# Kernel tuning notes

Hardware: AMD Instinct MI355X
Metric: run time of the kernel (lower is better)

The kernel has to match this reference:

```python
import jax, jax.numpy as jnp
import numpy as np

N_NODES = 50000
N_EDGES = 300000
HEADS = 2
OUT_CH = 128
BN_EPS = 1e-5
NEG_SLOPE = 0.2


def _batchnorm(x, g, b):
    # training-mode BatchNorm1d: biased batch statistics
    mean = x.mean(axis=0)
    var = x.var(axis=0)
    return (x - mean) * jax.lax.rsqrt(var + BN_EPS) * g + b


def _gatv2(x, src, dst, edge_attr, Wl, bl, Wr, br, We, att, bias, concat):
    # PyG GATv2Conv, share_weights=False, aggr='add'
    n = x.shape[0]
    xl = (x @ Wl + bl).reshape(n, HEADS, OUT_CH)  # source messages
    xr = (x @ Wr + br).reshape(n, HEADS, OUT_CH)  # destination term
    ee = (edge_attr @ We).reshape(-1, HEADS, OUT_CH)
    s = jax.nn.leaky_relu(xl[src] + xr[dst] + ee, NEG_SLOPE)  # [E,H,C]
    alpha = jnp.einsum('ehc,hc->eh', s, att)  # [E,H]
    # segment softmax over edges grouped by destination node
    m = jax.ops.segment_max(alpha, dst, num_segments=n)
    a = jnp.exp(alpha - m[dst])
    den = jax.ops.segment_sum(a, dst, num_segments=n)
    a = a / (den[dst] + 1e-16)
    out = jax.ops.segment_sum(xl[src] * a[:, :, None], dst, num_segments=n)  # [N,H,C]
    out = out.reshape(n, HEADS * OUT_CH) if concat else out.mean(axis=1)
    return out + bias


def setup_inputs() -> dict:
    key = jax.random.key(0)
    ks = jax.random.split(key, 16)
    d = {}
    d['h'] = jax.random.normal(ks[0], (N_NODES, 5), jnp.float32)
    d['edge_index'] = jax.random.randint(ks[1], (2, N_EDGES), 0, N_NODES, jnp.int64)
    d['edge_weight'] = jax.random.uniform(ks[2], (N_EDGES, 1), jnp.float32)
    d['bn0_g'] = jnp.ones((5,), jnp.float32)
    d['bn0_b'] = jnp.zeros((5,), jnp.float32)
    d['bn1_g'] = jnp.ones((256,), jnp.float32)
    d['bn1_b'] = jnp.zeros((256,), jnp.float32)
    def lin(k, fan_in, fan_out):
        return jax.random.normal(k, (fan_in, fan_out), jnp.float32) * (1.0 / np.sqrt(fan_in))
    # conv1: in=5 -> heads*out=256, concat=True
    d['c1_Wl'] = lin(ks[3], 5, 256); d['c1_bl'] = jnp.zeros((256,), jnp.float32)
    d['c1_Wr'] = lin(ks[4], 5, 256); d['c1_br'] = jnp.zeros((256,), jnp.float32)
    d['c1_We'] = lin(ks[5], 1, 256)
    d['c1_att'] = jax.random.normal(ks[6], (HEADS, OUT_CH), jnp.float32) * 0.1
    d['c1_bias'] = jnp.zeros((256,), jnp.float32)
    # mu: in=256 -> 128, concat=False
    d['mu_Wl'] = lin(ks[7], 256, 256); d['mu_bl'] = jnp.zeros((256,), jnp.float32)
    d['mu_Wr'] = lin(ks[8], 256, 256); d['mu_br'] = jnp.zeros((256,), jnp.float32)
    d['mu_We'] = lin(ks[9], 1, 256)
    d['mu_att'] = jax.random.normal(ks[10], (HEADS, OUT_CH), jnp.float32) * 0.1
    d['mu_bias'] = jnp.zeros((128,), jnp.float32)
    # log_std: same shapes as mu
    d['ls_Wl'] = lin(ks[11], 256, 256); d['ls_bl'] = jnp.zeros((256,), jnp.float32)
    d['ls_Wr'] = lin(ks[12], 256, 256); d['ls_br'] = jnp.zeros((256,), jnp.float32)
    d['ls_We'] = lin(ks[13], 1, 256)
    d['ls_att'] = jax.random.normal(ks[14], (HEADS, OUT_CH), jnp.float32) * 0.1
    d['ls_bias'] = jnp.zeros((128,), jnp.float32)
    return d


def reference(h, edge_index, edge_weight, bn0_g, bn0_b, bn1_g, bn1_b,
              c1_Wl, c1_bl, c1_Wr, c1_br, c1_We, c1_att, c1_bias,
              mu_Wl, mu_bl, mu_Wr, mu_br, mu_We, mu_att, mu_bias,
              ls_Wl, ls_bl, ls_Wr, ls_br, ls_We, ls_att, ls_bias):
    src, dst = edge_index[0], edge_index[1]
    x = _batchnorm(h, bn0_g, bn0_b)
    x = _gatv2(x, src, dst, edge_weight, c1_Wl, c1_bl, c1_Wr, c1_br, c1_We, c1_att, c1_bias, concat=True)
    x = jax.nn.relu(_batchnorm(x, bn1_g, bn1_b))
    # dropout identity (eval / deterministic)
    mu = _gatv2(x, src, dst, edge_weight, mu_Wl, mu_bl, mu_Wr, mu_br, mu_We, mu_att, mu_bias, concat=False)
    log_std = _gatv2(x, src, dst, edge_weight, ls_Wl, ls_bl, ls_Wr, ls_br, ls_We, ls_att, ls_bias, concat=False)
    return (mu, log_std)
```

## Files before the change

kernel.cpp:

```cpp
#include <hip/hip_runtime.h>
#include <math.h>

#define N_NODES 50000
#define N_EDGES 300000
#define BN_EPS 1e-5f
#define NEG_SLOPE 0.2f

#define RB_COUNT 3128
#define SCAN_TILES 49

typedef short bf8v __attribute__((ext_vector_type(8)));
typedef float f4v __attribute__((ext_vector_type(4)));

__device__ inline unsigned short f2bf(float f) {
    union { float f; unsigned u; } c; c.f = f;
    unsigned r = c.u + 0x7fffu + ((c.u >> 16) & 1u);
    return (unsigned short)(r >> 16);
}
__device__ inline float bf2f(unsigned short u) {
    union { unsigned u; float f; } c; c.u = ((unsigned)u) << 16;
    return c.f;
}

__device__ inline void async_copy16(void* lds, const void* g) {
    __builtin_amdgcn_global_load_lds(
        (const __attribute__((address_space(1))) unsigned int*)g,
        (__attribute__((address_space(3))) unsigned int*)lds, 16, 0, 0);
}

__global__ void bn0_reduce(const float* __restrict__ h, float* __restrict__ acc ) {
    __shared__ float lds[4][10];
    int tid = threadIdx.x;
    int lane = tid & 63, wave = tid >> 6;
    float ls[5] = {0,0,0,0,0}, lq[5] = {0,0,0,0,0};
    for (int r = blockIdx.x * 256 + tid; r < N_NODES; r += 128 * 256) {
        #pragma unroll
        for (int k = 0; k < 5; k++) {
            float v = h[r*5 + k];
            ls[k] += v; lq[k] += v*v;
        }
    }
    #pragma unroll
    for (int k = 0; k < 5; k++) {
        #pragma unroll
        for (int m = 1; m <= 32; m <<= 1) {
            ls[k] += __shfl_xor(ls[k], m, 64);
            lq[k] += __shfl_xor(lq[k], m, 64);
        }
    }
    if (lane == 0) {
        #pragma unroll
        for (int k = 0; k < 5; k++) { lds[wave][k] = ls[k]; lds[wave][5+k] = lq[k]; }
    }
    __syncthreads();
    if (tid < 10) {
        float s = lds[0][tid] + lds[1][tid] + lds[2][tid] + lds[3][tid];
        atomicAdd(&acc[tid], s);
    }
}

__global__ void bn0_finalize(const float* __restrict__ acc, const float* __restrict__ g,
                             const float* __restrict__ b, float* __restrict__ ss) {
    int tid = threadIdx.x;
    if (tid < 5) {
        float mean = acc[tid] * (1.f / N_NODES);
        float var  = acc[5 + tid] * (1.f / N_NODES) - mean*mean;
        float sc = g[tid] * rsqrtf(var + BN_EPS);
        ss[tid]     = sc;
        ss[5 + tid] = b[tid] - mean * sc;
    }
}

__global__ void bn0_apply(const float* __restrict__ h, const float* __restrict__ ss,
                          float* __restrict__ x0) {
    int i = blockIdx.x * blockDim.x + threadIdx.x;
    if (i < N_NODES * 5) {
        int k = i % 5;
        x0[i] = h[i] * ss[k] + ss[5 + k];
    }
}

__global__ void edge_count(const int* __restrict__ dst, int* __restrict__ count) {
    int e = blockIdx.x * blockDim.x + threadIdx.x;
    if (e < N_EDGES) atomicAdd(&count[dst[e]], 1);
}

__global__ void local_scan(const int* __restrict__ count, int* __restrict__ offsets,
                           int* __restrict__ tileSum) {
    __shared__ int lds[1024];
    int tid = threadIdx.x;
    int i = blockIdx.x * 1024 + tid;
    int v = (i < N_NODES) ? count[i] : 0;
    lds[tid] = v;
    __syncthreads();
    #pragma unroll
    for (int off = 1; off < 1024; off <<= 1) {
        int t = (tid >= off) ? lds[tid - off] : 0;
        __syncthreads();
        lds[tid] += t;
        __syncthreads();
    }
    if (i < N_NODES) offsets[i] = lds[tid] - v;
    if (tid == 1023) tileSum[blockIdx.x] = lds[1023];
}

__global__ void tile_scan(const int* __restrict__ tileSum, int* __restrict__ tilePrefix,
                          int* __restrict__ offsets) {
    int lane = threadIdx.x;
    int v = (lane < SCAN_TILES) ? tileSum[lane] : 0;
    int inc = v;
    #pragma unroll
    for (int off = 1; off < 64; off <<= 1) {
        int t = __shfl_up(inc, off, 64);
        if (lane >= off) inc += t;
    }
    int excl = inc - v;
    if (lane < SCAN_TILES) tilePrefix[lane] = excl;
    if (lane == SCAN_TILES - 1) offsets[N_NODES] = inc;
}

__global__ void add_prefix(int* __restrict__ offsets, const int* __restrict__ tilePrefix,
                           int* __restrict__ cursor) {
    int i = blockIdx.x * 1024 + threadIdx.x;
    if (i < N_NODES) {
        int o = offsets[i] + tilePrefix[blockIdx.x];
        offsets[i] = o;
        cursor[i] = o;
    }
}

__global__ void edge_scatter(const int* __restrict__ dst, const int* __restrict__ src,
                             const float* __restrict__ ew, int* __restrict__ cursor,
                             int* __restrict__ srcp, float* __restrict__ ewp) {
    int e = blockIdx.x * blockDim.x + threadIdx.x;
    if (e < N_EDGES) {
        int pos = atomicAdd(&cursor[dst[e]], 1);
        srcp[pos] = src[e];
        ewp[pos] = ew[e];
    }
}

__global__ void gemm_k5(const float* __restrict__ x0,
                        const float* __restrict__ Wl, const float* __restrict__ bl,
                        const float* __restrict__ Wr, const float* __restrict__ br,
                        unsigned short* __restrict__ xl, unsigned short* __restrict__ xr) {
    int n = blockIdx.x;
    int c = threadIdx.x;
    float a0 = x0[n*5+0], a1 = x0[n*5+1], a2 = x0[n*5+2], a3 = x0[n*5+3], a4 = x0[n*5+4];
    float l = bl[c] + a0*Wl[c] + a1*Wl[256+c] + a2*Wl[512+c] + a3*Wl[768+c] + a4*Wl[1024+c];
    float r = br[c] + a0*Wr[c] + a1*Wr[256+c] + a2*Wr[512+c] + a3*Wr[768+c] + a4*Wr[1024+c];
    xl[n*256 + c] = f2bf(l);
    xr[n*256 + c] = f2bf(r);
}

__global__ void pack_x_bn(const float* __restrict__ x,
                          const float* __restrict__ sum, const float* __restrict__ sumsq,
                          const float* __restrict__ g, const float* __restrict__ b,
                          unsigned short* __restrict__ ap) {
    int t = blockIdx.x * 256 + threadIdx.x;
    int lane = t & 63;
    int kc = (t >> 6) & 7;
    int rb = t >> 9;
    int row = rb * 16 + (lane & 15);
    int k0 = kc * 32 + (lane >> 4) * 8;
    union { unsigned short h[8]; uint4 u; } tmp;
    if (row < N_NODES) {
        const float* s = x + (size_t)row * 256 + k0;
        #pragma unroll
        for (int j = 0; j < 8; j++) {
            int c = k0 + j;
            float mean = sum[c] * (1.f / N_NODES);
            float var  = sumsq[c] * (1.f / N_NODES) - mean*mean;
            float sc = g[c] * rsqrtf(var + BN_EPS);
            float v = (s[j] - mean) * sc + b[c];
            v = v > 0.f ? v : 0.f;
            tmp.h[j] = f2bf(v);
        }
    } else {
        #pragma unroll
        for (int j = 0; j < 8; j++) tmp.h[j] = 0;
    }
    *reinterpret_cast<uint4*>(ap + (size_t)t * 8) = tmp.u;
}

__global__ void pack_w(const float* __restrict__ Wl0, const float* __restrict__ Wr0,
                       const float* __restrict__ Wl1, const float* __restrict__ Wr1,
                       unsigned short* __restrict__ bp) {
    int t = blockIdx.x * 256 + threadIdx.x;
    int lane = t & 63;
    int nt = (t >> 6) & 31;
    int kc = (t >> 11) & 7;
    int conv = t >> 14;
    int col = nt * 16 + (lane & 15);
    int k0 = kc * 32 + (lane >> 4) * 8;
    const float* W = conv ? (col < 256 ? Wl1 : Wr1) : (col < 256 ? Wl0 : Wr0);
    int c = col & 255;
    union { unsigned short h[8]; uint4 u; } tmp;
    #pragma unroll
    for (int j = 0; j < 8; j++) tmp.h[j] = f2bf(W[(size_t)(k0 + j) * 256 + c]);
    *reinterpret_cast<uint4*>(bp + (size_t)t * 8) = tmp.u;
}

__global__ __launch_bounds__(512) void gemm_mfma(const unsigned short* __restrict__ ap,
        const unsigned short* __restrict__ bp,
        const float* __restrict__ bl, const float* __restrict__ br,
        unsigned short* __restrict__ xl, unsigned short* __restrict__ xr) {
    __shared__ unsigned short Bs[2][32][512];
    int lane = threadIdx.x & 63;
    int wave = threadIdx.x >> 6;
    int h = wave & 1;
    int rb = blockIdx.x * 4 + (wave >> 1);

    const unsigned short* aptr = ap + (size_t)rb * 4096 + lane * 8;
    const unsigned short* bsrc = bp + lane * 8;

    auto stage = [&](int buf, int kc) {
        #pragma unroll
        for (int j = 0; j < 4; j++) {
            int f = wave * 4 + j;
            async_copy16(&Bs[buf][f][lane * 8], bsrc + (size_t)kc * 16384 + f * 512);
        }
    };
    stage(0, 0);

    bf8v a[8];
    #pragma unroll
    for (int kc = 0; kc < 8; kc++) a[kc] = *reinterpret_cast<const bf8v*>(aptr + kc * 512);

    f4v acc[16];
    #pragma unroll
    for (int t = 0; t < 16; t++) acc[t] = (f4v){0.f, 0.f, 0.f, 0.f};

    for (int kc = 0; kc < 8; kc++) {
        __syncthreads();
        if (kc < 7) stage((kc + 1) & 1, kc + 1);
        const unsigned short* bb = &Bs[kc & 1][h * 16][lane * 8];
        #pragma unroll
        for (int t = 0; t < 16; t++) {
            bf8v b = *reinterpret_cast<const bf8v*>(bb + t * 512);
            acc[t] = __builtin_amdgcn_mfma_f32_16x16x32_bf16(a[kc], b, acc[t], 0, 0, 0);
        }
    }

    int c15 = lane & 15;
    int row0 = rb * 16 + (lane >> 4) * 4;
    unsigned short* outp = h ? xr : xl;
    const float* bias = h ? br : bl;
    #pragma unroll
    for (int t = 0; t < 16; t++) {
        int col = t * 16 + c15;
        float bv = bias[col];
        #pragma unroll
        for (int r = 0; r < 4; r++) {
            int row = row0 + r;
            if (row < N_NODES) outp[(size_t)row * 256 + col] = f2bf(acc[t][r] + bv);
        }
    }
}

template <int CONCAT>
__global__ void agg_fused(const unsigned short* __restrict__ xl,
                          const unsigned short* __restrict__ xr,
                          const float* __restrict__ We, const float* __restrict__ att,
                          const int* __restrict__ offsets, const int* __restrict__ srcp,
                          const float* __restrict__ ewp, const float* __restrict__ bias,
                          float* __restrict__ out) {
    int n = blockIdx.x * 4 + (threadIdx.x >> 6);
    int lane = threadIdx.x & 63;
    if (n >= N_NODES) return;
    int col = (lane >> 5) * 128 + (lane & 31) * 4;
    float4 w4 = *(const float4*)(We + col);
    float4 a4 = *(const float4*)(att + col);
    ushort4 r4 = *(const ushort4*)(xr + (size_t)n * 256 + col);
    float rx = bf2f(r4.x), ry = bf2f(r4.y), rz = bf2f(r4.z), rw = bf2f(r4.w);
    int beg = offsets[n], end = offsets[n + 1];
    float mrun = -INFINITY, den = 0.f;
    float ax = 0.f, ay = 0.f, az = 0.f, aw = 0.f;
    for (int i = beg; i < end; i++) {
        int s = srcp[i];
        float w = ewp[i];
        ushort4 l4 = *(const ushort4*)(xl + (size_t)s * 256 + col);
        float lx = bf2f(l4.x), ly = bf2f(l4.y), lz = bf2f(l4.z), lw = bf2f(l4.w);
        float v, a = 0.f;
        v = lx + rx + w*w4.x; v = v > 0.f ? v : NEG_SLOPE*v; a += v*a4.x;
        v = ly + ry + w*w4.y; v = v > 0.f ? v : NEG_SLOPE*v; a += v*a4.y;
        v = lz + rz + w*w4.z; v = v > 0.f ? v : NEG_SLOPE*v; a += v*a4.z;
        v = lw + rw + w*w4.w; v = v > 0.f ? v : NEG_SLOPE*v; a += v*a4.w;
        #pragma unroll
        for (int mm = 1; mm <= 16; mm <<= 1) a += __shfl_xor(a, mm, 64);
        float nm = fmaxf(mrun, a);
        float sc = __expf(mrun - nm);
        float p  = __expf(a - nm);
        den = den * sc + p;
        ax = ax * sc + p * lx;
        ay = ay * sc + p * ly;
        az = az * sc + p * lz;
        aw = aw * sc + p * lw;
        mrun = nm;
    }
    float inv = 1.f / (den + 1e-16f);
    if (CONCAT) {
        float4 b4 = *(const float4*)(bias + col);
        float4 o;
        o.x = ax*inv + b4.x; o.y = ay*inv + b4.y; o.z = az*inv + b4.z; o.w = aw*inv + b4.w;
        *(float4*)(out + (size_t)n * 256 + col) = o;
    } else {
        float ox = ax*inv, oy = ay*inv, oz = az*inv, ow = aw*inv;
        float px = __shfl_xor(ox, 32, 64);
        float py = __shfl_xor(oy, 32, 64);
        float pz = __shfl_xor(oz, 32, 64);
        float pw = __shfl_xor(ow, 32, 64);
        if (lane < 32) {
            float4 b4 = *(const float4*)(bias + lane * 4);
            float4 o;
            o.x = (ox + px)*0.5f + b4.x;
            o.y = (oy + py)*0.5f + b4.y;
            o.z = (oz + pz)*0.5f + b4.z;
            o.w = (ow + pw)*0.5f + b4.w;
            *(float4*)(out + (size_t)n * 128 + lane * 4) = o;
        }
    }
}

__global__ void bn1_reduce(const float* __restrict__ x, float* __restrict__ sum,
                           float* __restrict__ sumsq) {
    int c = threadIdx.x;
    int r0 = blockIdx.x * 196;
    int r1 = r0 + 196; if (r1 > N_NODES) r1 = N_NODES;
    float s = 0.f, q = 0.f;
    for (int r = r0; r < r1; r++) {
        float v = x[r*256 + c];
        s += v; q += v*v;
    }
    atomicAdd(&sum[c], s);
    atomicAdd(&sumsq[c], q);
}

extern "C" void kernel_launch(void* const* d_in, const int* in_sizes, int n_in,
                              void* d_out, int out_size, void* d_ws, size_t ws_size,
                              hipStream_t stream) {
    const float* h          = (const float*)d_in[0];
    const int*   edge_index = (const int*)d_in[1];
    const int*   src = edge_index;
    const int*   dst = edge_index + N_EDGES;
    const float* ew   = (const float*)d_in[2];
    const float* bn0g = (const float*)d_in[3];
    const float* bn0b = (const float*)d_in[4];
    const float* bn1g = (const float*)d_in[5];
    const float* bn1b = (const float*)d_in[6];
    const float* c1_Wl = (const float*)d_in[7];
    const float* c1_bl = (const float*)d_in[8];
    const float* c1_Wr = (const float*)d_in[9];
    const float* c1_br = (const float*)d_in[10];
    const float* c1_We = (const float*)d_in[11];
    const float* c1_att = (const float*)d_in[12];
    const float* c1_bias = (const float*)d_in[13];
    const float* mu_Wl = (const float*)d_in[14];
    const float* mu_bl = (const float*)d_in[15];
    const float* mu_Wr = (const float*)d_in[16];
    const float* mu_br = (const float*)d_in[17];
    const float* mu_We = (const float*)d_in[18];
    const float* mu_att = (const float*)d_in[19];
    const float* mu_bias = (const float*)d_in[20];
    const float* ls_Wl = (const float*)d_in[21];
    const float* ls_bl = (const float*)d_in[22];
    const float* ls_Wr = (const float*)d_in[23];
    const float* ls_br = (const float*)d_in[24];
    const float* ls_We = (const float*)d_in[25];
    const float* ls_att = (const float*)d_in[26];
    const float* ls_bias = (const float*)d_in[27];

    float* out_mu = (float*)d_out;
    float* out_ls = (float*)d_out + (size_t)N_NODES * 128;

    char* ws = (char*)d_ws;
    size_t off = 0;
    auto alloc = [&](size_t bytes) -> void* {
        void* p = ws + off;
        off += (bytes + 255) / 256 * 256;
        return p;
    };
    float* x0      = (float*)alloc((size_t)N_NODES * 5 * 4);
    unsigned short* xl = (unsigned short*)alloc((size_t)N_NODES * 256 * 2);
    unsigned short* xr = (unsigned short*)alloc((size_t)N_NODES * 256 * 2);
    float* xB      = (float*)alloc((size_t)N_NODES * 256 * 4);
    float* bn0acc  = (float*)alloc(10 * 4);
    float* bn0ss   = (float*)alloc(10 * 4);
    float* bn1sum  = (float*)alloc(256 * 4);
    float* bn1sq   = (float*)alloc(256 * 4);
    int*   count   = (int*)alloc((size_t)N_NODES * 4);
    int*   offsets = (int*)alloc((size_t)(N_NODES + 1) * 4);
    int*   cursor  = (int*)alloc((size_t)N_NODES * 4);
    int*   srcp    = (int*)alloc((size_t)N_EDGES * 4);
    float* ewp     = (float*)alloc((size_t)N_EDGES * 4);
    int*   tileSum = (int*)alloc((size_t)SCAN_TILES * 4);
    int*   tilePre = (int*)alloc((size_t)SCAN_TILES * 4);
    unsigned short* Apack = (unsigned short*)alloc((size_t)RB_COUNT * 4096 * 2);
    unsigned short* Bpack = (unsigned short*)alloc((size_t)2 * 131072 * 2);

    hipMemsetAsync(count, 0, (size_t)N_NODES * 4, stream);
    hipMemsetAsync(bn0acc, 0, 10 * 4, stream);
    hipMemsetAsync(bn1sum, 0, 256 * 4, stream);
    hipMemsetAsync(bn1sq, 0, 256 * 4, stream);

    bn0_reduce<<<128, 256, 0, stream>>>(h, bn0acc);
    bn0_finalize<<<1, 64, 0, stream>>>(bn0acc, bn0g, bn0b, bn0ss);
    bn0_apply<<<(N_NODES * 5 + 255) / 256, 256, 0, stream>>>(h, bn0ss, x0);

    edge_count<<<(N_EDGES + 255) / 256, 256, 0, stream>>>(dst, count);
    local_scan<<<SCAN_TILES, 1024, 0, stream>>>(count, offsets, tileSum);
    tile_scan<<<1, 64, 0, stream>>>(tileSum, tilePre, offsets);
    add_prefix<<<SCAN_TILES, 1024, 0, stream>>>(offsets, tilePre, cursor);
    edge_scatter<<<(N_EDGES + 255) / 256, 256, 0, stream>>>(dst, src, ew, cursor, srcp, ewp);

    pack_w<<<128, 256, 0, stream>>>(mu_Wl, mu_Wr, ls_Wl, ls_Wr, Bpack);

    gemm_k5<<<N_NODES, 256, 0, stream>>>(x0, c1_Wl, c1_bl, c1_Wr, c1_br, xl, xr);
    agg_fused<1><<<N_NODES / 4 + 1, 256, 0, stream>>>(xl, xr, c1_We, c1_att, offsets,
                                                      srcp, ewp, c1_bias, xB);

    bn1_reduce<<<256, 256, 0, stream>>>(xB, bn1sum, bn1sq);
    pack_x_bn<<<6256, 256, 0, stream>>>(xB, bn1sum, bn1sq, bn1g, bn1b, Apack);

    gemm_mfma<<<782, 512, 0, stream>>>(Apack, Bpack, mu_bl, mu_br, xl, xr);
    agg_fused<0><<<N_NODES / 4 + 1, 256, 0, stream>>>(xl, xr, mu_We, mu_att, offsets,
                                                      srcp, ewp, mu_bias, out_mu);

    gemm_mfma<<<782, 512, 0, stream>>>(Apack, Bpack + 131072, ls_bl, ls_br, xl, xr);
    agg_fused<0><<<N_NODES / 4 + 1, 256, 0, stream>>>(xl, xr, ls_We, ls_att, offsets,
                                                      srcp, ewp, ls_bias, out_ls);
}
```

Baseline: 511.4 us.

## Split wave across two edges per iteration with 8-wide loads and prefetch

```diff
diff --git a/kernel.cpp b/kernel.cpp
--- a/kernel.cpp
+++ b/kernel.cpp
@@ -11,6 +11,7 @@
 
 typedef short bf8v __attribute__((ext_vector_type(8)));
 typedef float f4v __attribute__((ext_vector_type(4)));
+typedef unsigned short u8v __attribute__((ext_vector_type(8)));
 
 __device__ inline unsigned short f2bf(float f) {
     union { float f; unsigned u; } c; c.f = f;
@@ -268,56 +269,96 @@
     int n = blockIdx.x * 4 + (threadIdx.x >> 6);
     int lane = threadIdx.x & 63;
     if (n >= N_NODES) return;
-    int col = (lane >> 5) * 128 + (lane & 31) * 4;
-    float4 w4 = *(const float4*)(We + col);
-    float4 a4 = *(const float4*)(att + col);
-    ushort4 r4 = *(const ushort4*)(xr + (size_t)n * 256 + col);
-    float rx = bf2f(r4.x), ry = bf2f(r4.y), rz = bf2f(r4.z), rw = bf2f(r4.w);
+    int half = lane >> 5;
+    int sub  = lane & 31;
+    int cb   = (sub >> 4) * 128 + (sub & 15) * 8;
+    float wv[8], av[8], rv[8];
+    *(float4*)&wv[0] = *(const float4*)(We + cb);
+    *(float4*)&wv[4] = *(const float4*)(We + cb + 4);
+    *(float4*)&av[0] = *(const float4*)(att + cb);
+    *(float4*)&av[4] = *(const float4*)(att + cb + 4);
+    u8v r8 = *(const u8v*)(xr + (size_t)n * 256 + cb);
+    #pragma unroll
+    for (int j = 0; j < 8; j++) rv[j] = bf2f(r8[j]);
     int beg = offsets[n], end = offsets[n + 1];
-    float mrun = -INFINITY, den = 0.f;
-    float ax = 0.f, ay = 0.f, az = 0.f, aw = 0.f;
-    for (int i = beg; i < end; i++) {
-        int s = srcp[i];
-        float w = ewp[i];
-        ushort4 l4 = *(const ushort4*)(xl + (size_t)s * 256 + col);
-        float lx = bf2f(l4.x), ly = bf2f(l4.y), lz = bf2f(l4.z), lw = bf2f(l4.w);
-        float v, a = 0.f;
-        v = lx + rx + w*w4.x; v = v > 0.f ? v : NEG_SLOPE*v; a += v*a4.x;
-        v = ly + ry + w*w4.y; v = v > 0.f ? v : NEG_SLOPE*v; a += v*a4.y;
-        v = lz + rz + w*w4.z; v = v > 0.f ? v : NEG_SLOPE*v; a += v*a4.z;
-        v = lw + rw + w*w4.w; v = v > 0.f ? v : NEG_SLOPE*v; a += v*a4.w;
-        #pragma unroll
-        for (int mm = 1; mm <= 16; mm <<= 1) a += __shfl_xor(a, mm, 64);
+    float mrun = -1e30f, den = 0.f;
+    float acc[8];
+    #pragma unroll
+    for (int j = 0; j < 8; j++) acc[j] = 0.f;
+
+    int i = beg + half;
+    int sN = 0; float wN = 0.f;
+    u8v lN;
+    #pragma unroll
+    for (int j = 0; j < 8; j++) lN[j] = 0;
+    if (i < end) {
+        sN = srcp[i]; wN = ewp[i];
+        lN = *(const u8v*)(xl + (size_t)sN * 256 + cb);
+    }
+    for (; i < end; i += 2) {
+        u8v l8 = lN; float w = wN;
+        int nx = i + 2;
+        if (nx < end) {
+            sN = srcp[nx]; wN = ewp[nx];
+            lN = *(const u8v*)(xl + (size_t)sN * 256 + cb);
+        }
+        float lv[8];
+        float a = 0.f;
+        #pragma unroll
+        for (int j = 0; j < 8; j++) {
+            lv[j] = bf2f(l8[j]);
+            float v = lv[j] + rv[j] + w * wv[j];
+            v = fmaxf(v, NEG_SLOPE * v);
+            a += v * av[j];
+        }
+        a += __shfl_xor(a, 1, 64);
+        a += __shfl_xor(a, 2, 64);
+        a += __shfl_xor(a, 4, 64);
+        a += __shfl_xor(a, 8, 64);
         float nm = fmaxf(mrun, a);
-        float sc = __expf(mrun - nm);
-        float p  = __expf(a - nm);
-        den = den * sc + p;
-        ax = ax * sc + p * lx;
-        ay = ay * sc + p * ly;
-        az = az * sc + p * lz;
-        aw = aw * sc + p * lw;
+        float scl = __expf(mrun - nm);
+        float p = __expf(a - nm);
+        den = den * scl + p;
+        #pragma unroll
+        for (int j = 0; j < 8; j++) acc[j] = acc[j] * scl + p * lv[j];
         mrun = nm;
+    }
+    {
+        float mo  = __shfl_xor(mrun, 32, 64);
+        float dno = __shfl_xor(den, 32, 64);
+        float nm = fmaxf(mrun, mo);
+        float s0 = __expf(mrun - nm);
+        float s1 = __expf(mo - nm);
+        den = den * s0 + dno * s1;
+        #pragma unroll
+        for (int j = 0; j < 8; j++) {
+            float ao = __shfl_xor(acc[j], 32, 64);
+            acc[j] = acc[j] * s0 + ao * s1;
+        }
     }
     float inv = 1.f / (den + 1e-16f);
     if (CONCAT) {
-        float4 b4 = *(const float4*)(bias + col);
-        float4 o;
-        o.x = ax*inv + b4.x; o.y = ay*inv + b4.y; o.z = az*inv + b4.z; o.w = aw*inv + b4.w;
-        *(float4*)(out + (size_t)n * 256 + col) = o;
+        if (lane < 32) {
+            float o[8];
+            #pragma unroll
+            for (int j = 0; j < 8; j++) o[j] = acc[j] * inv + bias[cb + j];
+            *(float4*)(out + (size_t)n * 256 + cb)     = *(float4*)&o[0];
+            *(float4*)(out + (size_t)n * 256 + cb + 4) = *(float4*)&o[4];
+        }
     } else {
-        float ox = ax*inv, oy = ay*inv, oz = az*inv, ow = aw*inv;
-        float px = __shfl_xor(ox, 32, 64);
-        float py = __shfl_xor(oy, 32, 64);
-        float pz = __shfl_xor(oz, 32, 64);
-        float pw = __shfl_xor(ow, 32, 64);
-        if (lane < 32) {
-            float4 b4 = *(const float4*)(bias + lane * 4);
-            float4 o;
-            o.x = (ox + px)*0.5f + b4.x;
-            o.y = (oy + py)*0.5f + b4.y;
-            o.z = (oz + pz)*0.5f + b4.z;
-            o.w = (ow + pw)*0.5f + b4.w;
-            *(float4*)(out + (size_t)n * 128 + lane * 4) = o;
+        float o[8];
+        #pragma unroll
+        for (int j = 0; j < 8; j++) o[j] = acc[j] * inv;
+        float po[8];
+        #pragma unroll
+        for (int j = 0; j < 8; j++) po[j] = __shfl_xor(o[j], 16, 64);
+        if (lane < 16) {
+            int c0 = (lane & 15) * 8;
+            float r[8];
+            #pragma unroll
+            for (int j = 0; j < 8; j++) r[j] = (o[j] + po[j]) * 0.5f + bias[c0 + j];
+            *(float4*)(out + (size_t)n * 128 + c0)     = *(float4*)&r[0];
+            *(float4*)(out + (size_t)n * 128 + c0 + 4) = *(float4*)&r[4];
         }
     }
 }
```

Measured after the change: 469.4 us. 8.2% less time.
